# Performance work log

Hardware: AMD Instinct MI355X
Metric: run time of the kernel (lower is better)

Reference implementation:

```python
import jax, jax.numpy as jnp
import numpy as np

RES = 64            # resolution (patch side)
SIFTSCALE = 12.0
SQUARE = 1500.0     # maxWidth == maxHeight == W
PI = float(np.pi)


def setup_inputs() -> dict:
    key = jax.random.key(0)
    k1, k2, k3, k4 = jax.random.split(key, 4)
    B, H, W = 2048, 256, 256
    img = jax.random.uniform(k1, (B, 1, H, W), jnp.float32) * 255.0
    kpLoc = jax.random.uniform(k2, (B, 2), jnp.float32) * 1.2 - 0.6   # normalized kp location in [-0.6, 0.6]
    scaling = 0.5 + jax.random.uniform(k3, (B,), jnp.float32) * 1.5   # maxR = 6*scaling in [3, 12]
    rotation = jax.random.normal(k4, (B,), jnp.float32) * PI
    return {"img": img, "kpLoc": kpLoc, "scaling": scaling, "rotation": rotation}


def _grid_sample(img, grid):
    # bilinear, zeros padding, align_corners=False (torch F.grid_sample defaults)
    # img: [B,C,H,W], grid: [B,Hg,Wg,2] with (x, y) in [-1,1]
    B, C, H, W = img.shape
    x, y = grid[..., 0], grid[..., 1]
    ix = ((x + 1.0) * W - 1.0) * 0.5
    iy = ((y + 1.0) * H - 1.0) * 0.5
    ix0 = jnp.floor(ix); iy0 = jnp.floor(iy)
    wx1 = ix - ix0; wx0 = 1.0 - wx1
    wy1 = iy - iy0; wy0 = 1.0 - wy1
    imgf = img.reshape(B, C, H * W)
    Hg, Wg = x.shape[1], x.shape[2]

    def gather(ixf, iyf):
        valid = (ixf >= 0) & (ixf <= W - 1) & (iyf >= 0) & (iyf <= H - 1)
        ixc = jnp.clip(ixf, 0, W - 1).astype(jnp.int32)
        iyc = jnp.clip(iyf, 0, H - 1).astype(jnp.int32)
        flat = (iyc * W + ixc).reshape(B, 1, Hg * Wg)
        v = jnp.take_along_axis(imgf, flat, axis=2).reshape(B, C, Hg, Wg)
        return v * valid[:, None, :, :].astype(img.dtype)

    out = (gather(ix0, iy0) * (wx0 * wy0)[:, None]
           + gather(ix0 + 1, iy0) * (wx1 * wy0)[:, None]
           + gather(ix0, iy0 + 1) * (wx0 * wy1)[:, None]
           + gather(ix0 + 1, iy0 + 1) * (wx1 * wy1)[:, None])
    return out


def reference(img, kpLoc, scaling, rotation):
    B = img.shape[0]
    # identity affine_grid coords (align_corners=False): (2i+1)/R - 1
    xs = (jnp.arange(RES, dtype=jnp.float32) + 0.5) * (2.0 / RES) - 1.0
    gx = jnp.broadcast_to(xs[None, :], (RES, RES))   # grid[...,0]: varies along width  ("grid_y" in torch code)
    gy = jnp.broadcast_to(xs[:, None], (RES, RES))   # grid[...,1]: varies along height ("grid_x" in torch code)

    maxR = (0.5 * SIFTSCALE * scaling)[:, None, None]         # [B,1,1]
    normGrid = (gx + 1.0) * 0.5                                # in [0,1)
    r_s_ = jnp.exp(normGrid[None] * jnp.log(maxR))             # log-polar radius: maxR**normGrid
    r_s = (r_s_ - 1.0) / (maxR - 1.0) * (2.0 * maxR / SQUARE)  # W/maxWidth == 1
    t_s = (gy + 1.0)[None] * PI                                # angle in [0, 2pi)
    x_s = r_s * jnp.cos(t_s) + kpLoc[:, 0, None, None]
    y_s = r_s * jnp.sin(t_s) + kpLoc[:, 1, None, None]
    polargrid = jnp.stack((x_s, y_s), axis=-1)                 # [B,RES,RES,2]

    patches = _grid_sample(img, polargrid)                     # [B,1,RES,RES]

    # ptnOrient: circular roll along rows (angle axis) by rotation angle
    deg_per_px = 360.0 / RES
    n = jnp.mod(jnp.round(rotation * (180.0 / PI) / deg_per_px).astype(jnp.int32), RES)  # [B]
    rows = jnp.mod(jnp.arange(RES)[None, :] - n[:, None], RES)  # out[i] = patch[(i-n) mod RES]
    patches = jnp.take_along_axis(patches, rows[:, None, :, None], axis=2)
    return patches / 255.0
```

## Files before the change

kernel.cpp:

```cpp
#include <hip/hip_runtime.h>
#include <math.h>


#define RES 64
#define IMG_H 256
#define IMG_W 256

__global__ __launch_bounds__(256) void logpolar_kernel(
    const float* __restrict__ img,
    const float* __restrict__ kpLoc,
    const float* __restrict__ scaling,
    const float* __restrict__ rotation,
    float* __restrict__ out)
{
    const int idx   = blockIdx.x * 256 + threadIdx.x;
    const int b     = idx >> 12;
    const int local = idx & 4095;
    const int i     = local >> 6;
    const int j     = local & 63;

    const float scal = scaling[b];
    const float rot  = rotation[b];
    const float kx   = kpLoc[2 * b + 0];
    const float ky   = kpLoc[2 * b + 1];

    float t = rot * 57.295779513082323f;
    t = t / 5.625f;
    int n = (int)nearbyintf(t);
    n = ((n % RES) + RES) % RES;
    const int ip = (i - n + RES) & (RES - 1);

    const float xs_i = ((float)ip + 0.5f) * (2.0f / RES) - 1.0f;
    const float xs_j = ((float)j  + 0.5f) * (2.0f / RES) - 1.0f;

    const float maxR     = 6.0f * scal;
    const float normGrid = (xs_j + 1.0f) * 0.5f;
    const float r_s_     = expf(normGrid * logf(maxR));
    const float r_s      = (r_s_ - 1.0f) / (maxR - 1.0f) * ((2.0f * maxR) / 1500.0f);
    const float t_s      = (xs_i + 1.0f) * 3.14159265358979f;

    const float x_s = r_s * cosf(t_s) + kx;
    const float y_s = r_s * sinf(t_s) + ky;

    const float gx = ((x_s + 1.0f) * (float)IMG_W - 1.0f) * 0.5f;
    const float gy = ((y_s + 1.0f) * (float)IMG_H - 1.0f) * 0.5f;
    const float x0f = floorf(gx);
    const float y0f = floorf(gy);
    const float wx1 = gx - x0f, wx0 = 1.0f - wx1;
    const float wy1 = gy - y0f, wy0 = 1.0f - wy1;

    const float* __restrict__ imgb = img + (size_t)b * (IMG_H * IMG_W);

    auto sample = [&](float xf, float yf) -> float {
        bool valid = (xf >= 0.0f) & (xf <= (float)(IMG_W - 1)) &
                     (yf >= 0.0f) & (yf <= (float)(IMG_H - 1));
        int xc = (int)fminf(fmaxf(xf, 0.0f), (float)(IMG_W - 1));
        int yc = (int)fminf(fmaxf(yf, 0.0f), (float)(IMG_H - 1));
        float v = imgb[yc * IMG_W + xc];
        return valid ? v : 0.0f;
    };

    const float v00 = sample(x0f,        y0f);
    const float v10 = sample(x0f + 1.0f, y0f);
    const float v01 = sample(x0f,        y0f + 1.0f);
    const float v11 = sample(x0f + 1.0f, y0f + 1.0f);

    const float val = v00 * (wx0 * wy0) + v10 * (wx1 * wy0)
                    + v01 * (wx0 * wy1) + v11 * (wx1 * wy1);

    out[idx] = val / 255.0f;
}

extern "C" void kernel_launch(void* const* d_in, const int* in_sizes, int n_in,
                              void* d_out, int out_size, void* d_ws, size_t ws_size,
                              hipStream_t stream) {
    const float* img      = (const float*)d_in[0];
    const float* kpLoc    = (const float*)d_in[1];
    const float* scaling  = (const float*)d_in[2];
    const float* rotation = (const float*)d_in[3];
    float* out = (float*)d_out;

    const int total  = out_size;
    const int blocks = (total + 255) / 256;

    logpolar_kernel<<<blocks, 256, 0, stream>>>(img, kpLoc, scaling, rotation, out);
}
```

Baseline: 611.3 us.

## Precompute radial and angular tables in shared memory, one block per image

Restructures the kernel so each block handles one whole 64x64 patch. The 64 radii (exp/log) and 64 cos/sin values are computed once per block into shared memory rather than per output pixel. Each thread then loops over 16 outputs, doing only FMAs, bilinear gathers and a reciprocal multiply. This cuts transcendental work but adds a __syncthreads and gives fewer, longer-lived blocks. The kernel is likely bound by the scattered memory gathers, so the reduced arithmetic may matter little.

```diff
diff --git a/kernel.cpp b/kernel.cpp
--- a/kernel.cpp
+++ b/kernel.cpp
@@ -5,6 +5,7 @@
 #define RES 64
 #define IMG_H 256
 #define IMG_W 256
+#define PI_F 3.14159265358979f
 
 __global__ __launch_bounds__(256) void logpolar_kernel(
     const float* __restrict__ img,
@@ -13,62 +14,79 @@
     const float* __restrict__ rotation,
     float* __restrict__ out)
 {
-    const int idx   = blockIdx.x * 256 + threadIdx.x;
-    const int b     = idx >> 12;
-    const int local = idx & 4095;
-    const int i     = local >> 6;
-    const int j     = local & 63;
+    const int b = blockIdx.x;
+    const int t = threadIdx.x;
+
+    __shared__ float s_r[RES];
+    __shared__ float s_c[RES];
+    __shared__ float s_s[RES];
 
     const float scal = scaling[b];
     const float rot  = rotation[b];
     const float kx   = kpLoc[2 * b + 0];
     const float ky   = kpLoc[2 * b + 1];
+    const float maxR = 6.0f * scal;
 
-    float t = rot * 57.295779513082323f;
-    t = t / 5.625f;
-    int n = (int)nearbyintf(t);
-    n = ((n % RES) + RES) % RES;
-    const int ip = (i - n + RES) & (RES - 1);
+    if (t < RES) {
+        const float xs_j     = ((float)t + 0.5f) * (2.0f / RES) - 1.0f;
+        const float normGrid = (xs_j + 1.0f) * 0.5f;
+        const float r_       = expf(normGrid * logf(maxR));
+        s_r[t] = (r_ - 1.0f) / (maxR - 1.0f) * ((2.0f * maxR) / 1500.0f);
+    } else if (t < 2 * RES) {
+        const int k = t - RES;
+        const float xs  = ((float)k + 0.5f) * (2.0f / RES) - 1.0f;
+        const float ang = (xs + 1.0f) * PI_F;
+        s_c[k] = cosf(ang);
+        s_s[k] = sinf(ang);
+    }
+    __syncthreads();
 
-    const float xs_i = ((float)ip + 0.5f) * (2.0f / RES) - 1.0f;
-    const float xs_j = ((float)j  + 0.5f) * (2.0f / RES) - 1.0f;
+    float tt = rot * 57.295779513082323f;
+    tt = tt / 5.625f;
+    int n = (int)nearbyintf(tt);
+    n = ((n % RES) + RES) & (RES - 1);
 
-    const float maxR     = 6.0f * scal;
-    const float normGrid = (xs_j + 1.0f) * 0.5f;
-    const float r_s_     = expf(normGrid * logf(maxR));
-    const float r_s      = (r_s_ - 1.0f) / (maxR - 1.0f) * ((2.0f * maxR) / 1500.0f);
-    const float t_s      = (xs_i + 1.0f) * 3.14159265358979f;
+    const float rj = s_r[t & (RES - 1)];
+    const float* __restrict__ imgb = img + (size_t)b * (IMG_H * IMG_W);
+    float* __restrict__ outb = out + (size_t)b * (RES * RES);
 
-    const float x_s = r_s * cosf(t_s) + kx;
-    const float y_s = r_s * sinf(t_s) + ky;
+    #pragma unroll
+    for (int k = 0; k < 16; ++k) {
+        const int idx = k * 256 + t;
+        const int i   = idx >> 6;
+        const int ip  = (i - n + RES) & (RES - 1);
+        const float c = s_c[ip];
+        const float s = s_s[ip];
 
-    const float gx = ((x_s + 1.0f) * (float)IMG_W - 1.0f) * 0.5f;
-    const float gy = ((y_s + 1.0f) * (float)IMG_H - 1.0f) * 0.5f;
-    const float x0f = floorf(gx);
-    const float y0f = floorf(gy);
-    const float wx1 = gx - x0f, wx0 = 1.0f - wx1;
-    const float wy1 = gy - y0f, wy0 = 1.0f - wy1;
+        const float x_s = fmaf(rj, c, kx);
+        const float y_s = fmaf(rj, s, ky);
 
-    const float* __restrict__ imgb = img + (size_t)b * (IMG_H * IMG_W);
+        const float gx = fmaf(x_s, 128.0f, 127.5f);
+        const float gy = fmaf(y_s, 128.0f, 127.5f);
+        const float x0f = floorf(gx);
+        const float y0f = floorf(gy);
+        const float wx1 = gx - x0f, wx0 = 1.0f - wx1;
+        const float wy1 = gy - y0f, wy0 = 1.0f - wy1;
 
-    auto sample = [&](float xf, float yf) -> float {
-        bool valid = (xf >= 0.0f) & (xf <= (float)(IMG_W - 1)) &
-                     (yf >= 0.0f) & (yf <= (float)(IMG_H - 1));
-        int xc = (int)fminf(fmaxf(xf, 0.0f), (float)(IMG_W - 1));
-        int yc = (int)fminf(fmaxf(yf, 0.0f), (float)(IMG_H - 1));
-        float v = imgb[yc * IMG_W + xc];
-        return valid ? v : 0.0f;
-    };
+        auto sample = [&](float xf, float yf) -> float {
+            bool valid = (xf >= 0.0f) & (xf <= (float)(IMG_W - 1)) &
+                         (yf >= 0.0f) & (yf <= (float)(IMG_H - 1));
+            int xc = (int)fminf(fmaxf(xf, 0.0f), (float)(IMG_W - 1));
+            int yc = (int)fminf(fmaxf(yf, 0.0f), (float)(IMG_H - 1));
+            float v = imgb[yc * IMG_W + xc];
+            return valid ? v : 0.0f;
+        };
 
-    const float v00 = sample(x0f,        y0f);
-    const float v10 = sample(x0f + 1.0f, y0f);
-    const float v01 = sample(x0f,        y0f + 1.0f);
-    const float v11 = sample(x0f + 1.0f, y0f + 1.0f);
+        const float v00 = sample(x0f,        y0f);
+        const float v10 = sample(x0f + 1.0f, y0f);
+        const float v01 = sample(x0f,        y0f + 1.0f);
+        const float v11 = sample(x0f + 1.0f, y0f + 1.0f);
 
-    const float val = v00 * (wx0 * wy0) + v10 * (wx1 * wy0)
-                    + v01 * (wx0 * wy1) + v11 * (wx1 * wy1);
+        const float val = v00 * (wx0 * wy0) + v10 * (wx1 * wy0)
+                        + v01 * (wx0 * wy1) + v11 * (wx1 * wy1);
 
-    out[idx] = val / 255.0f;
+        outb[idx] = val * (1.0f / 255.0f);
+    }
 }
 
 extern "C" void kernel_launch(void* const* d_in, const int* in_sizes, int n_in,
@@ -80,8 +98,6 @@
     const float* rotation = (const float*)d_in[3];
     float* out = (float*)d_out;
 
-    const int total  = out_size;
-    const int blocks = (total + 255) / 256;
-
-    logpolar_kernel<<<blocks, 256, 0, stream>>>(img, kpLoc, scaling, rotation, out);
+    const int B = in_sizes[2];
+    logpolar_kernel<<<B, 256, 0, stream>>>(img, kpLoc, scaling, rotation, out);
 }
```

Measured after the change: 592.6 us. 1.03x faster.
